# Kernel tuning notes

Measured on AMD Instinct MI355X. Metric: run time of the kernel, lower is better.

## Reference

```python
import jax, jax.numpy as jnp
import numpy as np

B_SZ, L, D_MODEL = 2, 2048, 2048
INTER, HEADS, P, N, G, K = 4096, 64, 64, 128, 1, 4
CONV_DIM = INTER + 2 * G * N
EPS = 1e-5


def silu(x):
    return x * jax.nn.sigmoid(x)


def softplus_thresh(x, threshold=10.0):
    # matches source: where(x < thr, log(1+exp(x)), x)
    return jnp.where(x < threshold, jnp.log1p(jnp.exp(jnp.minimum(x, threshold))), x)


def setup_inputs() -> dict:
    key = jax.random.key(0)
    ks = jax.random.split(key, 8)
    s = 0.02
    return {
        "hidden_states": jax.random.normal(ks[0], (B_SZ, L, D_MODEL), jnp.float32),
        "W_z": jax.random.normal(ks[1], (D_MODEL, INTER), jnp.float32) * s,
        "W_xBC": jax.random.normal(ks[2], (D_MODEL, CONV_DIM), jnp.float32) * s,
        "W_dt": jax.random.normal(ks[3], (D_MODEL, HEADS), jnp.float32) * s,
        "conv_w": jax.random.normal(ks[4], (CONV_DIM, K), jnp.float32) * 0.1,
        "conv_b": jnp.zeros((CONV_DIM,), jnp.float32),
        "dt_bias": jax.random.uniform(ks[5], (HEADS,), jnp.float32, -2.0, 0.0),
        "A_log": jnp.log(jnp.arange(1, HEADS + 1, dtype=jnp.float32)),
        "D": jnp.ones((HEADS,), jnp.float32),
        "norm_w": jnp.ones((INTER,), jnp.float32),
        "W_out": jax.random.normal(ks[6], (INTER, D_MODEL), jnp.float32) * s,
    }


def reference(hidden_states, W_z, W_xBC, W_dt, conv_w, conv_b, dt_bias, A_log, D, norm_w, W_out):
    b, l, _ = hidden_states.shape
    Hg = HEADS // G  # heads per group

    gate = hidden_states @ W_z                      # [b,l,INTER]
    xBC = hidden_states @ W_xBC                     # [b,l,CONV_DIM]
    dt = softplus_thresh(hidden_states @ W_dt + dt_bias)  # [b,l,H]

    # causal depthwise conv1d + silu (padding=K-1, truncated to seq_len)
    xp = jnp.pad(xBC, ((0, 0), (K - 1, 0), (0, 0)))
    kern = jnp.transpose(conv_w)[:, None, :]        # [K,1,CONV_DIM] (WIO)
    xBC = jax.lax.conv_general_dilated(
        xp, kern, (1,), 'VALID',
        dimension_numbers=('NWC', 'WIO', 'NWC'),
        feature_group_count=CONV_DIM)
    xBC = silu(xBC + conv_b)

    gns = G * N
    x = xBC[..., :INTER].reshape(b, l, G, Hg, P)
    Bm = xBC[..., INTER:INTER + gns].reshape(b, l, G, N)
    Cm = xBC[..., INTER + gns:].reshape(b, l, G, N)

    A = -jnp.exp(A_log)                             # [H]
    dA = jnp.exp(dt * A).reshape(b, l, G, Hg)       # [b,l,G,Hg]
    dtx = dt.reshape(b, l, G, Hg)[..., None] * x    # [b,l,G,Hg,P]

    def step(state, inp):
        dA_t, dtx_t, B_t, C_t = inp
        # state: [b,G,Hg,P,N]
        state = state * dA_t[..., None, None] + dtx_t[..., None] * B_t[:, :, None, None, :]
        y_t = jnp.einsum('bghpn,bgn->bghp', state, C_t)
        return state, y_t

    xs = (jnp.moveaxis(dA, 1, 0), jnp.moveaxis(dtx, 1, 0),
          jnp.moveaxis(Bm, 1, 0), jnp.moveaxis(Cm, 1, 0))
    state0 = jnp.zeros((b, G, Hg, P, N), jnp.float32)
    _, ys = jax.lax.scan(step, state0, xs)          # [l,b,G,Hg,P]
    y = jnp.moveaxis(ys, 0, 1) + D.reshape(G, Hg)[..., None] * x
    scan_out = y.reshape(b, l, INTER)

    # gated RMSNorm within groups
    hs = scan_out.reshape(b, l, G, INTER // G).astype(jnp.float32)
    gt = gate.reshape(b, l, G, INTER // G).astype(jnp.float32)
    hs = hs * silu(gt)
    var = jnp.mean(hs * hs, axis=-1, keepdims=True)
    hs = hs * jax.lax.rsqrt(var + EPS)
    normed = norm_w * hs.reshape(b, l, INTER)

    return normed @ W_out
```

## Files before the change

### kernel.cpp

```cpp
#include <hip/hip_runtime.h>
#include <hip/hip_bf16.h>
#include <math.h>

typedef unsigned short u16;
typedef unsigned int   u32;
typedef __attribute__((ext_vector_type(8))) short short8;
typedef __attribute__((ext_vector_type(4))) float f32x4;

#define B_SZ     2
#define LSEQ     2048
#define DMODEL   2048
#define INTER    4096
#define HEADS    64
#define NSTATE   128
#define CONV_DIM 4352
#define XSTR     8576
#define NFUSE    8704
#define EPS      1e-5f
#define QCH      64
#define NCHUNK   (LSEQ / QCH)

__device__ __forceinline__ float bf2f(u16 u) {
    u32 v = ((u32)u) << 16;
    return __builtin_bit_cast(float, v);
}
__device__ __forceinline__ u16 f2bf(float x) {
    __hip_bfloat16 h = __float2bfloat16(x);
    return __builtin_bit_cast(u16, h);
}
__device__ __forceinline__ u32 pack2(float lo, float hi) {
    return (u32)f2bf(lo) | ((u32)f2bf(hi) << 16);
}
__device__ __forceinline__ void gl2lds16(const void* g, void* l) {
    __builtin_amdgcn_global_load_lds(
        (const __attribute__((address_space(1))) u32*)g,
        (__attribute__((address_space(3))) u32*)l, 16, 0, 0);
}

__global__ __launch_bounds__(256) void cvt_f32_bf16(
    const float* __restrict__ in, u16* __restrict__ out, int n4)
{
    int i = blockIdx.x * 256 + threadIdx.x;
    if (i >= n4) return;
    float4 v = ((const float4*)in)[i];
    ushort4 o;
    o.x = f2bf(v.x); o.y = f2bf(v.y); o.z = f2bf(v.z); o.w = f2bf(v.w);
    ((ushort4*)out)[i] = o;
}

__global__ __launch_bounds__(256) void tr_f32_bf16(
    const float* __restrict__ in, u16* __restrict__ out, int R, int C)
{
    __shared__ u16 tile[64][68];
    const int r0 = blockIdx.y * 64, c0 = blockIdx.x * 64;
    const int tr = threadIdx.x >> 4, tc = (threadIdx.x & 15) * 4;
    #pragma unroll
    for (int i = 0; i < 4; ++i) {
        int r = tr + i * 16;
        float4 v = *(const float4*)(in + (size_t)(r0 + r) * C + c0 + tc);
        tile[r][tc + 0] = f2bf(v.x);
        tile[r][tc + 1] = f2bf(v.y);
        tile[r][tc + 2] = f2bf(v.z);
        tile[r][tc + 3] = f2bf(v.w);
    }
    __syncthreads();
    #pragma unroll
    for (int i = 0; i < 4; ++i) {
        int oc = tr + i * 16;
        ushort4 o;
        o.x = tile[tc + 0][oc];
        o.y = tile[tc + 1][oc];
        o.z = tile[tc + 2][oc];
        o.w = tile[tc + 3][oc];
        *(ushort4*)(out + (size_t)(c0 + oc) * R + r0 + tc) = o;
    }
}

#define SA(c) (smem + (c) * 32768)
#define SB(c) (smem + (c) * 32768 + 16384)
#define STGA(c, q, ko) gl2lds16(gA + (size_t)((q) * 64) * lda + (ko), SA(c) + (q) * 4096 + lbase)
#define STGB(c, q, ko) gl2lds16(gB + (size_t)((q) * 64) * ldb + (ko), SB(c) + (q) * 4096 + lbase)

#define PH(mh, kk, READB, STAGES, TAIL)                                          \
  {                                                                              \
    short8 af[4];                                                                \
    _Pragma("unroll")                                                            \
    for (int i_ = 0; i_ < 4; ++i_)                                               \
      af[i_] = *(const short8*)(Ab + (wm * 128 + (mh) * 64 + i_ * 16 + lr) * 64  \
                                + ((((kk) * 4 + lq) ^ (lr & 7)) << 3));          \
    if (READB) {                                                                 \
      _Pragma("unroll")                                                          \
      for (int j_ = 0; j_ < 4; ++j_)                                             \
        bfr[kk][j_] = *(const short8*)(Bb + (wn * 64 + j_ * 16 + lr) * 64        \
                                       + ((((kk) * 4 + lq) ^ (lr & 7)) << 3));   \
    }                                                                            \
    STAGES                                                                       \
    __builtin_amdgcn_sched_barrier(0);                                           \
    __builtin_amdgcn_s_barrier();                                                \
    asm volatile("s_waitcnt lgkmcnt(0)" ::: "memory");                           \
    __builtin_amdgcn_sched_barrier(0);                                           \
    __builtin_amdgcn_s_setprio(1);                                               \
    _Pragma("unroll")                                                            \
    for (int i_ = 0; i_ < 4; ++i_)                                               \
      _Pragma("unroll")                                                          \
      for (int j_ = 0; j_ < 4; ++j_)                                             \
        acc[(mh) * 4 + i_][j_] = __builtin_amdgcn_mfma_f32_16x16x32_bf16(        \
            af[i_], bfr[kk][j_], acc[(mh) * 4 + i_][j_], 0, 0, 0);               \
    __builtin_amdgcn_s_setprio(0);                                               \
    __builtin_amdgcn_sched_barrier(0);                                           \
    TAIL                                                                         \
    __builtin_amdgcn_s_barrier();                                                \
  }

#define TILE(tt, c)                                                              \
  {                                                                              \
    const int t_ = (tt);                                                         \
    const int k1_ = (t_ + 1) << 6, k2_ = (t_ + 2) << 6;                          \
    const bool st1_ = (t_ + 1 < nt), st2_ = (t_ + 2 < nt);                       \
    const u16* Ab = SA(c); const u16* Bb = SB(c);                                \
    PH(0, 0, 1, { if (st1_) { STGA((c) ^ 1, 1, k1_); STGA((c) ^ 1, 3, k1_); } }, {}) \
    PH(1, 0, 0, { if (st1_) { STGB((c) ^ 1, 0, k1_); STGB((c) ^ 1, 1, k1_); } }, {}) \
    PH(0, 1, 1, { if (st1_) { STGB((c) ^ 1, 2, k1_); STGB((c) ^ 1, 3, k1_); } }, {}) \
    PH(1, 1, 0, { if (st2_) { STGA((c), 0, k2_); STGA((c), 2, k2_); } },         \
       { if (t_ < nt - 1) {                                                      \
           if (st2_) { asm volatile("s_waitcnt vmcnt(2)" ::: "memory"); }        \
           else      { asm volatile("s_waitcnt vmcnt(0)" ::: "memory"); } } })   \
  }

template<int OUT_BF16>
__global__ __launch_bounds__(512, 2) void gemm8(
    const u16* __restrict__ A, const u16* __restrict__ Bt, void* __restrict__ Co,
    int K, int lda, int ldb, int ldc, int Nstore)
{
    __shared__ __align__(16) u16 smem[65536];
    const int tid  = threadIdx.x;
    const int wave = tid >> 6, lane = tid & 63;
    const int wm = wave >> 2, wn = wave & 3;
    const int lr = lane & 15, lq = lane >> 4;

    const int nbx = gridDim.x;
    const int bid = blockIdx.y * nbx + blockIdx.x;
    const int nwg = nbx * gridDim.y;
    const int cpx = nwg >> 3;
    const int swz = (bid & 7) * cpx + (bid >> 3);
    const int n0 = (swz % nbx) * 256;
    const int m0 = (swz / nbx) * 256;
    const int kbase = blockIdx.z * K;

    const int srow  = tid >> 3;
    const int scb8  = ((tid & 7) ^ (srow & 7)) << 3;
    const int lbase = (tid >> 6) << 9;
    const u16* gA = A  + (size_t)(m0 + srow) * lda + kbase + scb8;
    const u16* gB = Bt + (size_t)(n0 + srow) * ldb + kbase + scb8;

    f32x4 acc[8][4];
    #pragma unroll
    for (int i = 0; i < 8; ++i)
        #pragma unroll
        for (int j = 0; j < 4; ++j) acc[i][j] = (f32x4)0.f;
    short8 bfr[2][4];

    const int nt = K >> 6;

    STGA(0, 0, 0); STGA(0, 1, 0); STGA(0, 2, 0); STGA(0, 3, 0);
    STGB(0, 0, 0); STGB(0, 1, 0); STGB(0, 2, 0); STGB(0, 3, 0);
    STGA(1, 0, 64); STGA(1, 2, 64);
    __builtin_amdgcn_sched_barrier(0);
    asm volatile("s_waitcnt vmcnt(2)" ::: "memory");
    __builtin_amdgcn_sched_barrier(0);
    __builtin_amdgcn_s_barrier();

    for (int t = 0; t < nt; t += 2) {
        TILE(t, 0)
        TILE(t + 1, 1)
    }

    const int odd = lr & 1;
    const bool wstore = (n0 + wn * 64) < Nstore;
    #pragma unroll
    for (int i = 0; i < 8; ++i)
        #pragma unroll
        for (int j = 0; j < 4; ++j) {
            float v0 = acc[i][j][0], v1 = acc[i][j][1];
            float v2 = acc[i][j][2], v3 = acc[i][j][3];
            float n0v = __shfl_xor(v0, 1), n1v = __shfl_xor(v1, 1);
            float n2v = __shfl_xor(v2, 1), n3v = __shfl_xor(v3, 1);
            int colb  = n0 + wn * 64 + j * 16 + (lr & ~1);
            int rbase = m0 + wm * 128 + i * 16 + lq * 4 + odd * 2;
            if (wstore) {
                if (OUT_BF16) {
                    u32 w0 = odd ? pack2(n2v, v2) : pack2(v0, n0v);
                    u32 w1 = odd ? pack2(n3v, v3) : pack2(v1, n1v);
                    *(u32*)((u16*)Co + (size_t)rbase * ldc + colb) = w0;
                    *(u32*)((u16*)Co + (size_t)(rbase + 1) * ldc + colb) = w1;
                } else {
                    float* Cf = (float*)Co + (size_t)blockIdx.z * 4096 * ldc;
                    float2 f0 = odd ? make_float2(n2v, v2) : make_float2(v0, n0v);
                    float2 f1 = odd ? make_float2(n3v, v3) : make_float2(v1, n1v);
                    *(float2*)(Cf + (size_t)rbase * ldc + colb) = f0;
                    *(float2*)(Cf + (size_t)(rbase + 1) * ldc + colb) = f1;
                }
            }
        }
}

__global__ __launch_bounds__(256) void add2_f32(
    const float* __restrict__ a, const float* __restrict__ b,
    float* __restrict__ o, int n4)
{
    int i = blockIdx.x * 256 + threadIdx.x;
    if (i >= n4) return;
    float4 x = ((const float4*)a)[i];
    float4 y = ((const float4*)b)[i];
    x.x += y.x; x.y += y.y; x.z += y.z; x.w += y.w;
    ((float4*)o)[i] = x;
}

__global__ void dt_kernel(const u16* __restrict__ xall,
                          float* __restrict__ dtb,
                          const float* __restrict__ dt_bias, int n)
{
    int i = blockIdx.x * 256 + threadIdx.x;
    if (i >= n) return;
    int h = i & 63, row = i >> 6;
    float x = bf2f(xall[(size_t)row * XSTR + INTER + CONV_DIM + h]) + dt_bias[h];
    dtb[i] = (x < 10.f) ? log1pf(expf(x)) : x;
}

__global__ void conv_kernel(const u16* __restrict__ xall,
                            const float* __restrict__ cw,
                            const float* __restrict__ cb,
                            u16* __restrict__ xout)
{
    int c  = blockIdx.x * 256 + threadIdx.x;
    int bt = blockIdx.y;
    int t  = bt & (LSEQ - 1);
    const u16* xi = xall + (size_t)bt * XSTR + INTER + c;
    float4 w = *(const float4*)(cw + (size_t)c * 4);
    float acc = cb[c];
    acc = fmaf(bf2f(xi[0]), w.w, acc);
    if (t >= 1) acc = fmaf(bf2f(*(xi - XSTR)),     w.z, acc);
    if (t >= 2) acc = fmaf(bf2f(*(xi - 2 * XSTR)), w.y, acc);
    if (t >= 3) acc = fmaf(bf2f(*(xi - 3 * XSTR)), w.x, acc);
    xout[(size_t)bt * CONV_DIM + c] = f2bf(acc / (1.f + expf(-acc)));
}

__global__ __launch_bounds__(256) void ssd_chunk_state(
    const u16* __restrict__ xc, const float* __restrict__ dtb,
    const float* __restrict__ A_log,
    u16* __restrict__ Tg, float* __restrict__ decayQ)
{
    const int bid = blockIdx.x;
    const int b = bid >> 11, h = (bid >> 5) & 63, c = bid & 31;
    const int t0 = c * QCH;
    const int tid = threadIdx.x;
    const int wave = tid >> 6, lane = tid & 63;
    const int lr = lane & 15, lq = lane >> 4;

    __shared__ __align__(16) u16 BT[128][72];
    __shared__ __align__(16) u16 XwT[64][72];
    __shared__ float sclL[QCH];

    const u16* xg = xc + (size_t)b * LSEQ * CONV_DIM;

    if (tid < 64) {
        float dtv = dtb[((size_t)b * LSEQ + t0 + tid) * HEADS + h];
        float a = -dtv * expf(A_log[h]);
        float s = a;
        #pragma unroll
        for (int off = 1; off < 64; off <<= 1) {
            float o = __shfl_up(s, off, 64);
            if (tid >= off) s += o;
        }
        float cq = __shfl(s, 63, 64);
        sclL[tid] = dtv * expf(cq - s);
        if (tid == 0) decayQ[((b * 64 + h) << 5) + c] = expf(cq);
    }
    __syncthreads();

    #pragma unroll
    for (int r = 0; r < 16; ++r) {
        int idx = tid + 256 * r, j = idx >> 6, p = idx & 63;
        float v = bf2f(xg[(size_t)(t0 + j) * CONV_DIM + h * 64 + p]);
        XwT[p][j] = f2bf(v * sclL[j]);
    }
    #pragma unroll
    for (int r = 0; r < 32; ++r) {
        int idx = tid + 256 * r, j = idx >> 7, n = idx & 127;
        BT[n][j] = xg[(size_t)(t0 + j) * CONV_DIM + INTER + n];
    }
    __syncthreads();

    f32x4 acc[8];
    #pragma unroll
    for (int i = 0; i < 8; ++i) acc[i] = (f32x4)0.f;
    #pragma unroll
    for (int k0 = 0; k0 < QCH; k0 += 32) {
        short8 af = *(const short8*)&XwT[wave * 16 + lr][k0 + lq * 8];
        #pragma unroll
        for (int nt = 0; nt < 8; ++nt) {
            short8 bfr = *(const short8*)&BT[nt * 16 + lr][k0 + lq * 8];
            acc[nt] = __builtin_amdgcn_mfma_f32_16x16x32_bf16(af, bfr, acc[nt], 0, 0, 0);
        }
    }
    u16* To = Tg + ((((size_t)(b * 64 + h)) * NCHUNK + c) * 64) * 128;
    #pragma unroll
    for (int nt = 0; nt < 8; ++nt)
        #pragma unroll
        for (int r = 0; r < 4; ++r)
            To[(wave * 16 + lq * 4 + r) * 128 + nt * 16 + lr] = f2bf(acc[nt][r]);
}

__global__ __launch_bounds__(256) void ssd_state_scan(
    u16* __restrict__ Tg, const float* __restrict__ decayQ)
{
    const int bh = blockIdx.x, tid = threadIdx.x;
    const int p = tid >> 2, nb = (tid & 3) * 32;
    float S[32];
    #pragma unroll
    for (int m = 0; m < 32; ++m) S[m] = 0.f;

    for (int c = 0; c < NCHUNK; ++c) {
        u16* base = Tg + ((((size_t)bh * NCHUNK + c) * 64 + p) * 128) + nb;
        uint4 tv[4];
        #pragma unroll
        for (int k = 0; k < 4; ++k) tv[k] = *(const uint4*)(base + k * 8);
        #pragma unroll
        for (int k = 0; k < 4; ++k) {
            uint4 sv;
            sv.x = pack2(S[k*8+0], S[k*8+1]);
            sv.y = pack2(S[k*8+2], S[k*8+3]);
            sv.z = pack2(S[k*8+4], S[k*8+5]);
            sv.w = pack2(S[k*8+6], S[k*8+7]);
            *(uint4*)(base + k * 8) = sv;
        }
        float dq = decayQ[(bh << 5) + c];
        #pragma unroll
        for (int k = 0; k < 4; ++k) {
            const u32* w = (const u32*)&tv[k];
            #pragma unroll
            for (int e = 0; e < 4; ++e) {
                S[k*8 + e*2]     = fmaf(dq, S[k*8 + e*2],     bf2f((u16)(w[e] & 0xffffu)));
                S[k*8 + e*2 + 1] = fmaf(dq, S[k*8 + e*2 + 1], bf2f((u16)(w[e] >> 16)));
            }
        }
    }
}

__global__ __launch_bounds__(256) void ssd_output(
    const u16* __restrict__ xc, const float* __restrict__ dtb,
    const float* __restrict__ A_log, const float* __restrict__ Dvec,
    const u16* __restrict__ Sg,
    u16* __restrict__ y)
{
    const int bid = blockIdx.x;
    const int b = bid >> 11, h = (bid >> 5) & 63, c = bid & 31;
    const int t0 = c * QCH;
    const int tid = threadIdx.x;
    const int wave = tid >> 6, lane = tid & 63;
    const int lr = lane & 15, lq = lane >> 4;

    __shared__ __align__(16) u16 C_lds[64][136];
    __shared__ __align__(16) u16 B_lds[64][136];
    __shared__ __align__(16) u16 S_lds[64][136];
    __shared__ __align__(16) u16 P_lds[64][72];
    __shared__ __align__(16) u16 XT[64][72];
    __shared__ float cumL[QCH], dtsL[QCH], escL[QCH];

    const u16* xg = xc + (size_t)b * LSEQ * CONV_DIM;

    if (tid < 64) {
        float dtv = dtb[((size_t)b * LSEQ + t0 + tid) * HEADS + h];
        float a = -dtv * expf(A_log[h]);
        float s = a;
        #pragma unroll
        for (int off = 1; off < 64; off <<= 1) {
            float o = __shfl_up(s, off, 64);
            if (tid >= off) s += o;
        }
        cumL[tid] = s;
        dtsL[tid] = dtv;
        escL[tid] = expf(s);
    }
    #pragma unroll
    for (int r4 = 0; r4 < 4; ++r4) {
        int idx4 = tid + 256 * r4;
        int j = idx4 >> 4, c8 = (idx4 & 15) * 8;
        *(uint4*)&B_lds[j][c8] = *(const uint4*)(xg + (size_t)(t0 + j) * CONV_DIM + INTER + c8);
        *(uint4*)&C_lds[j][c8] = *(const uint4*)(xg + (size_t)(t0 + j) * CONV_DIM + INTER + NSTATE + c8);
        *(uint4*)&S_lds[j][c8] = *(const uint4*)(Sg + ((((size_t)(b * 64 + h)) * NCHUNK + c) * 64 + j) * 128 + c8);
    }
    #pragma unroll
    for (int r = 0; r < 16; ++r) {
        int idx = tid + 256 * r, j = idx >> 6, p = idx & 63;
        XT[p][j] = xg[(size_t)(t0 + j) * CONV_DIM + h * 64 + p];
    }
    __syncthreads();

    f32x4 accG[4];
    #pragma unroll
    for (int i = 0; i < 4; ++i) accG[i] = (f32x4)0.f;
    #pragma unroll
    for (int k0 = 0; k0 < NSTATE; k0 += 32) {
        short8 af = *(const short8*)&C_lds[wave * 16 + lr][k0 + lq * 8];
        #pragma unroll
        for (int jt = 0; jt < 4; ++jt) {
            short8 bfr = *(const short8*)&B_lds[jt * 16 + lr][k0 + lq * 8];
            accG[jt] = __builtin_amdgcn_mfma_f32_16x16x32_bf16(af, bfr, accG[jt], 0, 0, 0);
        }
    }
    #pragma unroll
    for (int jt = 0; jt < 4; ++jt)
        #pragma unroll
        for (int r = 0; r < 4; ++r) {
            int ii = wave * 16 + lq * 4 + r;
            int jj = jt * 16 + lr;
            float v = (jj <= ii)
                ? accG[jt][r] * dtsL[jj] * expf(cumL[ii] - cumL[jj]) : 0.f;
            P_lds[ii][jj] = f2bf(v);
        }
    __syncthreads();

    f32x4 accY[4], accZ[4];
    #pragma unroll
    for (int i = 0; i < 4; ++i) { accY[i] = (f32x4)0.f; accZ[i] = (f32x4)0.f; }
    #pragma unroll
    for (int k0 = 0; k0 < QCH; k0 += 32) {
        short8 af = *(const short8*)&P_lds[wave * 16 + lr][k0 + lq * 8];
        #pragma unroll
        for (int pt = 0; pt < 4; ++pt) {
            short8 bfr = *(const short8*)&XT[pt * 16 + lr][k0 + lq * 8];
            accY[pt] = __builtin_amdgcn_mfma_f32_16x16x32_bf16(af, bfr, accY[pt], 0, 0, 0);
        }
    }
    #pragma unroll
    for (int k0 = 0; k0 < NSTATE; k0 += 32) {
        short8 af = *(const short8*)&C_lds[wave * 16 + lr][k0 + lq * 8];
        #pragma unroll
        for (int pt = 0; pt < 4; ++pt) {
            short8 bfr = *(const short8*)&S_lds[pt * 16 + lr][k0 + lq * 8];
            accZ[pt] = __builtin_amdgcn_mfma_f32_16x16x32_bf16(af, bfr, accZ[pt], 0, 0, 0);
        }
    }

    const float Dh = Dvec[h];
    u16* yg = y + ((size_t)b * LSEQ + t0) * XSTR + h * 64;
    #pragma unroll
    for (int pt = 0; pt < 4; ++pt)
        #pragma unroll
        for (int r = 0; r < 4; ++r) {
            int ii = wave * 16 + lq * 4 + r;
            int pp = pt * 16 + lr;
            float xv = bf2f(XT[pp][ii]);
            float o = accY[pt][r] + escL[ii] * accZ[pt][r] + Dh * xv;
            yg[(size_t)ii * XSTR + pp] = f2bf(o);
        }
}

__global__ __launch_bounds__(256) void norm_kernel(
    u16* __restrict__ xall, const float* __restrict__ w)
{
    const int row = blockIdx.x;
    const u16* yr = xall + (size_t)row * XSTR + INTER;
    u16*       gr = xall + (size_t)row * XSTR;
    const int tid = threadIdx.x;

    float v[16];
    float ss = 0.f;
    #pragma unroll
    for (int i = 0; i < 16; ++i) {
        int idx = tid + i * 256;
        float hv = bf2f(yr[idx]);
        float g  = bf2f(gr[idx]);
        float val = hv * (g / (1.f + expf(-g)));
        v[i] = val;
        ss = fmaf(val, val, ss);
    }
    #pragma unroll
    for (int o = 32; o > 0; o >>= 1) ss += __shfl_xor(ss, o);
    __shared__ float part[4];
    if ((tid & 63) == 0) part[tid >> 6] = ss;
    __syncthreads();
    float tot  = part[0] + part[1] + part[2] + part[3];
    float rinv = rsqrtf(tot * (1.f / INTER) + EPS);
    #pragma unroll
    for (int i = 0; i < 16; ++i) {
        int idx = tid + i * 256;
        gr[idx] = f2bf(w[idx] * v[i] * rinv);
    }
}

extern "C" void kernel_launch(void* const* d_in, const int* in_sizes, int n_in,
                              void* d_out, int out_size, void* d_ws, size_t ws_size,
                              hipStream_t stream)
{
    const float* hs      = (const float*)d_in[0];
    const float* W_z     = (const float*)d_in[1];
    const float* W_xBC   = (const float*)d_in[2];
    const float* W_dt    = (const float*)d_in[3];
    const float* conv_w  = (const float*)d_in[4];
    const float* conv_b  = (const float*)d_in[5];
    const float* dt_bias = (const float*)d_in[6];
    const float* A_log   = (const float*)d_in[7];
    const float* Dv      = (const float*)d_in[8];
    const float* norm_w  = (const float*)d_in[9];
    const float* W_out   = (const float*)d_in[10];
    float* out = (float*)d_out;
    char*  w8  = (char*)d_ws;

    u16* hs_bf  = (u16*)(w8 + 0);
    u16* Wt_all = (u16*)(w8 + 16777216);
    u16* Tbuf   = (u16*)(w8 + 0);
    float* Cpart= (float*)(w8 + 0);
    u16* Wt_out = (u16*)(w8 + 67108864);
    u16* xall   = (u16*)(w8 + 83886080);
    u16* xconv  = (u16*)(w8 + 154140672);
    float* dtb  = (float*)(w8 + 189792256);
    float* dcq  = (float*)(w8 + 190840832);

    const int M = B_SZ * LSEQ;

    cvt_f32_bf16<<<(M * DMODEL / 4 + 255) / 256, 256, 0, stream>>>(hs, hs_bf, M * DMODEL / 4);
    tr_f32_bf16<<<dim3(INTER / 64,    DMODEL / 64), 256, 0, stream>>>(W_z,   Wt_all, DMODEL, INTER);
    tr_f32_bf16<<<dim3(CONV_DIM / 64, DMODEL / 64), 256, 0, stream>>>(W_xBC, Wt_all + (size_t)INTER * DMODEL, DMODEL, CONV_DIM);
    tr_f32_bf16<<<dim3(1,             DMODEL / 64), 256, 0, stream>>>(W_dt,  Wt_all + (size_t)(INTER + CONV_DIM) * DMODEL, DMODEL, 64);
    hipMemsetAsync(Wt_all + (size_t)(INTER + CONV_DIM + 64) * DMODEL, 0, (size_t)192 * DMODEL * 2, stream);
    tr_f32_bf16<<<dim3(DMODEL / 64,   INTER / 64),  256, 0, stream>>>(W_out, Wt_out, INTER, DMODEL);

    gemm8<1><<<dim3(NFUSE / 256, M / 256, 1), 512, 0, stream>>>(
        hs_bf, Wt_all, (void*)xall, DMODEL , DMODEL , DMODEL ,
        XSTR , XSTR );

    dt_kernel<<<(M * HEADS + 255) / 256, 256, 0, stream>>>(xall, dtb, dt_bias, M * HEADS);
    conv_kernel<<<dim3(CONV_DIM / 256, M), 256, 0, stream>>>(xall, conv_w, conv_b, xconv);

    ssd_chunk_state<<<B_SZ * HEADS * NCHUNK, 256, 0, stream>>>(xconv, dtb, A_log, Tbuf, dcq);
    ssd_state_scan<<<B_SZ * HEADS, 256, 0, stream>>>(Tbuf, dcq);
    ssd_output<<<B_SZ * HEADS * NCHUNK, 256, 0, stream>>>(xconv, dtb, A_log, Dv, Tbuf, xall + INTER);

    norm_kernel<<<M, 256, 0, stream>>>(xall, norm_w);

    gemm8<0><<<dim3(DMODEL / 256, M / 256, 2), 512, 0, stream>>>(
        xall, Wt_out, (void*)Cpart, INTER / 2 , XSTR ,
        INTER , DMODEL , DMODEL );
    add2_f32<<<(M * DMODEL / 4 + 255) / 256, 256, 0, stream>>>(
        Cpart, Cpart + (size_t)M * DMODEL, out, M * DMODEL / 4);
}
```

Baseline: 638.6 us.

## Replace 256x256x64 GEMM with 128x256x32 double-buffered kernel at higher occupancy

The two bf16 GEMMs move from a 256x256 tile with 64-wide K steps and a phased four-stage LDS pipeline to a 128x256 tile with 32-wide K steps. The new kernel uses a simple two-buffer LDS ring of 48KB and launch bounds allowing four blocks per CU. The aim is more resident waves and more blocks in flight to hide latency, at the cost of lower arithmetic intensity per tile and more barriers per unit of K. The XOR swizzle on LDS reads is dropped, which may bring bank conflicts back.

```diff
diff --git a/kernel.cpp b/kernel.cpp
--- a/kernel.cpp
+++ b/kernel.cpp
@@ -76,63 +76,12 @@
     }
 }
 
-#define SA(c) (smem + (c) * 32768)
-#define SB(c) (smem + (c) * 32768 + 16384)
-#define STGA(c, q, ko) gl2lds16(gA + (size_t)((q) * 64) * lda + (ko), SA(c) + (q) * 4096 + lbase)
-#define STGB(c, q, ko) gl2lds16(gB + (size_t)((q) * 64) * ldb + (ko), SB(c) + (q) * 4096 + lbase)
-
-#define PH(mh, kk, READB, STAGES, TAIL)                                          \
-  {                                                                              \
-    short8 af[4];                                                                \
-    _Pragma("unroll")                                                            \
-    for (int i_ = 0; i_ < 4; ++i_)                                               \
-      af[i_] = *(const short8*)(Ab + (wm * 128 + (mh) * 64 + i_ * 16 + lr) * 64  \
-                                + ((((kk) * 4 + lq) ^ (lr & 7)) << 3));          \
-    if (READB) {                                                                 \
-      _Pragma("unroll")                                                          \
-      for (int j_ = 0; j_ < 4; ++j_)                                             \
-        bfr[kk][j_] = *(const short8*)(Bb + (wn * 64 + j_ * 16 + lr) * 64        \
-                                       + ((((kk) * 4 + lq) ^ (lr & 7)) << 3));   \
-    }                                                                            \
-    STAGES                                                                       \
-    __builtin_amdgcn_sched_barrier(0);                                           \
-    __builtin_amdgcn_s_barrier();                                                \
-    asm volatile("s_waitcnt lgkmcnt(0)" ::: "memory");                           \
-    __builtin_amdgcn_sched_barrier(0);                                           \
-    __builtin_amdgcn_s_setprio(1);                                               \
-    _Pragma("unroll")                                                            \
-    for (int i_ = 0; i_ < 4; ++i_)                                               \
-      _Pragma("unroll")                                                          \
-      for (int j_ = 0; j_ < 4; ++j_)                                             \
-        acc[(mh) * 4 + i_][j_] = __builtin_amdgcn_mfma_f32_16x16x32_bf16(        \
-            af[i_], bfr[kk][j_], acc[(mh) * 4 + i_][j_], 0, 0, 0);               \
-    __builtin_amdgcn_s_setprio(0);                                               \
-    __builtin_amdgcn_sched_barrier(0);                                           \
-    TAIL                                                                         \
-    __builtin_amdgcn_s_barrier();                                                \
-  }
-
-#define TILE(tt, c)                                                              \
-  {                                                                              \
-    const int t_ = (tt);                                                         \
-    const int k1_ = (t_ + 1) << 6, k2_ = (t_ + 2) << 6;                          \
-    const bool st1_ = (t_ + 1 < nt), st2_ = (t_ + 2 < nt);                       \
-    const u16* Ab = SA(c); const u16* Bb = SB(c);                                \
-    PH(0, 0, 1, { if (st1_) { STGA((c) ^ 1, 1, k1_); STGA((c) ^ 1, 3, k1_); } }, {}) \
-    PH(1, 0, 0, { if (st1_) { STGB((c) ^ 1, 0, k1_); STGB((c) ^ 1, 1, k1_); } }, {}) \
-    PH(0, 1, 1, { if (st1_) { STGB((c) ^ 1, 2, k1_); STGB((c) ^ 1, 3, k1_); } }, {}) \
-    PH(1, 1, 0, { if (st2_) { STGA((c), 0, k2_); STGA((c), 2, k2_); } },         \
-       { if (t_ < nt - 1) {                                                      \
-           if (st2_) { asm volatile("s_waitcnt vmcnt(2)" ::: "memory"); }        \
-           else      { asm volatile("s_waitcnt vmcnt(0)" ::: "memory"); } } })   \
-  }
-
 template<int OUT_BF16>
-__global__ __launch_bounds__(512, 2) void gemm8(
+__global__ __launch_bounds__(512, 4) void gemmk(
     const u16* __restrict__ A, const u16* __restrict__ Bt, void* __restrict__ Co,
     int K, int lda, int ldb, int ldc, int Nstore)
 {
-    __shared__ __align__(16) u16 smem[65536];
+    __shared__ __align__(16) u16 smem[2][12288];
     const int tid  = threadIdx.x;
     const int wave = tid >> 6, lane = tid & 63;
     const int wm = wave >> 2, wn = wave & 3;
@@ -144,41 +93,86 @@
     const int cpx = nwg >> 3;
     const int swz = (bid & 7) * cpx + (bid >> 3);
     const int n0 = (swz % nbx) * 256;
-    const int m0 = (swz / nbx) * 256;
+    const int m0 = (swz / nbx) * 128;
     const int kbase = blockIdx.z * K;
 
-    const int srow  = tid >> 3;
-    const int scb8  = ((tid & 7) ^ (srow & 7)) << 3;
-    const int lbase = (tid >> 6) << 9;
-    const u16* gA = A  + (size_t)(m0 + srow) * lda + kbase + scb8;
-    const u16* gB = Bt + (size_t)(n0 + srow) * ldb + kbase + scb8;
-
-    f32x4 acc[8][4];
-    #pragma unroll
-    for (int i = 0; i < 8; ++i)
+    const int lbase = wave << 9;
+    const u16* gA = A  + (size_t)(m0 + (tid >> 2)) * lda + kbase + (tid & 3) * 8;
+    const u16* gB = Bt + (size_t)(n0 + (tid >> 2)) * ldb + kbase + (tid & 3) * 8;
+
+    f32x4 acc[4][4];
+    #pragma unroll
+    for (int i = 0; i < 4; ++i)
         #pragma unroll
         for (int j = 0; j < 4; ++j) acc[i][j] = (f32x4)0.f;
-    short8 bfr[2][4];
-
-    const int nt = K >> 6;
-
-    STGA(0, 0, 0); STGA(0, 1, 0); STGA(0, 2, 0); STGA(0, 3, 0);
-    STGB(0, 0, 0); STGB(0, 1, 0); STGB(0, 2, 0); STGB(0, 3, 0);
-    STGA(1, 0, 64); STGA(1, 2, 64);
+
+    const int nt = K >> 5;
+
+    gl2lds16(gA,                  &smem[0][0]    + lbase);
+    gl2lds16(gB,                  &smem[0][4096] + lbase);
+    gl2lds16(gB + (size_t)128 * ldb, &smem[0][8192] + lbase);
+    gl2lds16(gA + 32,                &smem[1][0]    + lbase);
+    gl2lds16(gB + 32,                &smem[1][4096] + lbase);
+    gl2lds16(gB + (size_t)128 * ldb + 32, &smem[1][8192] + lbase);
     __builtin_amdgcn_sched_barrier(0);
-    asm volatile("s_waitcnt vmcnt(2)" ::: "memory");
+    asm volatile("s_waitcnt vmcnt(3)" ::: "memory");
     __builtin_amdgcn_sched_barrier(0);
     __builtin_amdgcn_s_barrier();
 
-    for (int t = 0; t < nt; t += 2) {
-        TILE(t, 0)
-        TILE(t + 1, 1)
+    const u16* gA2 = gA + 64;
+    const u16* gB2 = gB + 64;
+
+    for (int t = 0; t < nt; ++t) {
+        const int c = t & 1;
+        const u16* Ab = &smem[c][0];
+        const u16* Bb = &smem[c][4096];
+        short8 af0 = *(const short8*)(Ab + (wm * 64 +  0 + lr) * 32 + lq * 8);
+        short8 af1 = *(const short8*)(Ab + (wm * 64 + 16 + lr) * 32 + lq * 8);
+        short8 bfr[4];
+        #pragma unroll
+        for (int j = 0; j < 4; ++j)
+            bfr[j] = *(const short8*)(Bb + (wn * 64 + j * 16 + lr) * 32 + lq * 8);
+        short8 af2 = *(const short8*)(Ab + (wm * 64 + 32 + lr) * 32 + lq * 8);
+        short8 af3 = *(const short8*)(Ab + (wm * 64 + 48 + lr) * 32 + lq * 8);
+        __builtin_amdgcn_s_setprio(1);
+        #pragma unroll
+        for (int j = 0; j < 4; ++j) {
+            acc[0][j] = __builtin_amdgcn_mfma_f32_16x16x32_bf16(af0, bfr[j], acc[0][j], 0, 0, 0);
+            acc[1][j] = __builtin_amdgcn_mfma_f32_16x16x32_bf16(af1, bfr[j], acc[1][j], 0, 0, 0);
+        }
+        __builtin_amdgcn_s_setprio(0);
+        asm volatile("s_waitcnt lgkmcnt(0)" ::: "memory");
+        __builtin_amdgcn_sched_barrier(0);
+        __builtin_amdgcn_s_barrier();
+
+        const bool st2 = (t + 2 < nt);
+        if (st2) {
+            gl2lds16(gA2,                  &smem[c][0]    + lbase);
+            gl2lds16(gB2,                  &smem[c][4096] + lbase);
+            gl2lds16(gB2 + (size_t)128 * ldb, &smem[c][8192] + lbase);
+            gA2 += 32; gB2 += 32;
+        }
+        __builtin_amdgcn_sched_barrier(0);
+        __builtin_amdgcn_s_setprio(1);
+        #pragma unroll
+        for (int j = 0; j < 4; ++j) {
+            acc[2][j] = __builtin_amdgcn_mfma_f32_16x16x32_bf16(af2, bfr[j], acc[2][j], 0, 0, 0);
+            acc[3][j] = __builtin_amdgcn_mfma_f32_16x16x32_bf16(af3, bfr[j], acc[3][j], 0, 0, 0);
+        }
+        __builtin_amdgcn_s_setprio(0);
+        __builtin_amdgcn_sched_barrier(0);
+        if (st2) {
+            asm volatile("s_waitcnt vmcnt(3)" ::: "memory");
+        } else if (t + 1 < nt) {
+            asm volatile("s_waitcnt vmcnt(0)" ::: "memory");
+        }
+        __builtin_amdgcn_s_barrier();
     }
 
     const int odd = lr & 1;
     const bool wstore = (n0 + wn * 64) < Nstore;
     #pragma unroll
-    for (int i = 0; i < 8; ++i)
+    for (int i = 0; i < 4; ++i)
         #pragma unroll
         for (int j = 0; j < 4; ++j) {
             float v0 = acc[i][j][0], v1 = acc[i][j][1];
@@ -186,7 +180,7 @@
             float n0v = __shfl_xor(v0, 1), n1v = __shfl_xor(v1, 1);
             float n2v = __shfl_xor(v2, 1), n3v = __shfl_xor(v3, 1);
             int colb  = n0 + wn * 64 + j * 16 + (lr & ~1);
-            int rbase = m0 + wm * 128 + i * 16 + lq * 4 + odd * 2;
+            int rbase = m0 + wm * 64 + i * 16 + lq * 4 + odd * 2;
             if (wstore) {
                 if (OUT_BF16) {
                     u32 w0 = odd ? pack2(n2v, v2) : pack2(v0, n0v);
@@ -527,7 +521,7 @@
     hipMemsetAsync(Wt_all + (size_t)(INTER + CONV_DIM + 64) * DMODEL, 0, (size_t)192 * DMODEL * 2, stream);
     tr_f32_bf16<<<dim3(DMODEL / 64,   INTER / 64),  256, 0, stream>>>(W_out, Wt_out, INTER, DMODEL);
 
-    gemm8<1><<<dim3(NFUSE / 256, M / 256, 1), 512, 0, stream>>>(
+    gemmk<1><<<dim3(NFUSE / 256, M / 128, 1), 512, 0, stream>>>(
         hs_bf, Wt_all, (void*)xall, DMODEL , DMODEL , DMODEL ,
         XSTR , XSTR );
 
@@ -540,7 +534,7 @@
 
     norm_kernel<<<M, 256, 0, stream>>>(xall, norm_w);
 
-    gemm8<0><<<dim3(DMODEL / 256, M / 256, 2), 512, 0, stream>>>(
+    gemmk<0><<<dim3(DMODEL / 256, M / 128, 2), 512, 0, stream>>>(
         xall, Wt_out, (void*)Cpart, INTER / 2 , XSTR ,
         INTER , DMODEL , DMODEL );
     add2_f32<<<(M * DMODEL / 4 + 255) / 256, 256, 0, stream>>>(
```

Result: slower. 672.1 us (+5.2%).

## Split-K the projection GEMM tail and parallelize state scan across N quarters

Applied to the files above, without the earlier changes.

The fused input-projection GEMM is split into a main 8192-column part and a 512-column tail. The tail (the last xBC, dt and padding columns) runs as a 4-way split-K fp32 GEMM and is reduced into bf16 by a new tail_add kernel, which is meant to cut the wave-quantization cost of the partial last column tile. Separately, ssd_state_scan now launches 4x more blocks, each handling 8 state elements per thread instead of 32, to expose more parallelism in the sequential chunk scan. The change adds two extra launches and an fp32 partial buffer that aliases the xconv region.

```diff
diff --git a/kernel.cpp b/kernel.cpp
--- a/kernel.cpp
+++ b/kernel.cpp
@@ -15,7 +15,9 @@
 #define NSTATE   128
 #define CONV_DIM 4352
 #define XSTR     8576
-#define NFUSE    8704
+#define NMAIN    8192
+#define NTAILC   512
+#define NTAILS   384
 #define EPS      1e-5f
 #define QCH      64
 #define NCHUNK   (LSEQ / QCH)
@@ -204,6 +206,25 @@
         }
 }
 
+__global__ __launch_bounds__(256) void tail_add(
+    const float* __restrict__ Pt, u16* __restrict__ xall_)
+{
+    int i = blockIdx.x * 256 + threadIdx.x;
+    int row = i / 96, cq = (i % 96) * 4;
+    const float* p = Pt + (size_t)row * NTAILC + cq;
+    const size_t zs = (size_t)4096 * NTAILC;
+    float4 a = *(const float4*)(p);
+    float4 b = *(const float4*)(p + zs);
+    float4 c = *(const float4*)(p + 2 * zs);
+    float4 d = *(const float4*)(p + 3 * zs);
+    ushort4 o;
+    o.x = f2bf(a.x + b.x + c.x + d.x);
+    o.y = f2bf(a.y + b.y + c.y + d.y);
+    o.z = f2bf(a.z + b.z + c.z + d.z);
+    o.w = f2bf(a.w + b.w + c.w + d.w);
+    *(ushort4*)(xall_ + (size_t)row * XSTR + NMAIN + cq) = o;
+}
+
 __global__ __launch_bounds__(256) void add2_f32(
     const float* __restrict__ a, const float* __restrict__ b,
     float* __restrict__ o, int n4)
@@ -314,35 +335,28 @@
 __global__ __launch_bounds__(256) void ssd_state_scan(
     u16* __restrict__ Tg, const float* __restrict__ decayQ)
 {
-    const int bh = blockIdx.x, tid = threadIdx.x;
-    const int p = tid >> 2, nb = (tid & 3) * 32;
-    float S[32];
-    #pragma unroll
-    for (int m = 0; m < 32; ++m) S[m] = 0.f;
+    const int bh = blockIdx.x >> 2, nq = blockIdx.x & 3;
+    const int tid = threadIdx.x;
+    const int p = tid >> 2, nb = nq * 32 + (tid & 3) * 8;
+    float S[8];
+    #pragma unroll
+    for (int m = 0; m < 8; ++m) S[m] = 0.f;
 
     for (int c = 0; c < NCHUNK; ++c) {
         u16* base = Tg + ((((size_t)bh * NCHUNK + c) * 64 + p) * 128) + nb;
-        uint4 tv[4];
-        #pragma unroll
-        for (int k = 0; k < 4; ++k) tv[k] = *(const uint4*)(base + k * 8);
-        #pragma unroll
-        for (int k = 0; k < 4; ++k) {
-            uint4 sv;
-            sv.x = pack2(S[k*8+0], S[k*8+1]);
-            sv.y = pack2(S[k*8+2], S[k*8+3]);
-            sv.z = pack2(S[k*8+4], S[k*8+5]);
-            sv.w = pack2(S[k*8+6], S[k*8+7]);
-            *(uint4*)(base + k * 8) = sv;
-        }
+        uint4 tv = *(const uint4*)base;
+        uint4 sv;
+        sv.x = pack2(S[0], S[1]);
+        sv.y = pack2(S[2], S[3]);
+        sv.z = pack2(S[4], S[5]);
+        sv.w = pack2(S[6], S[7]);
+        *(uint4*)base = sv;
         float dq = decayQ[(bh << 5) + c];
-        #pragma unroll
-        for (int k = 0; k < 4; ++k) {
-            const u32* w = (const u32*)&tv[k];
-            #pragma unroll
-            for (int e = 0; e < 4; ++e) {
-                S[k*8 + e*2]     = fmaf(dq, S[k*8 + e*2],     bf2f((u16)(w[e] & 0xffffu)));
-                S[k*8 + e*2 + 1] = fmaf(dq, S[k*8 + e*2 + 1], bf2f((u16)(w[e] >> 16)));
-            }
+        const u32* w = (const u32*)&tv;
+        #pragma unroll
+        for (int e = 0; e < 4; ++e) {
+            S[e*2]     = fmaf(dq, S[e*2],     bf2f((u16)(w[e] & 0xffffu)));
+            S[e*2 + 1] = fmaf(dq, S[e*2 + 1], bf2f((u16)(w[e] >> 16)));
         }
     }
 }
@@ -515,6 +529,7 @@
     u16* Wt_out = (u16*)(w8 + 67108864);
     u16* xall   = (u16*)(w8 + 83886080);
     u16* xconv  = (u16*)(w8 + 154140672);
+    float* Ptail= (float*)(w8 + 154140672);
     float* dtb  = (float*)(w8 + 189792256);
     float* dcq  = (float*)(w8 + 190840832);
 
@@ -527,15 +542,19 @@
     hipMemsetAsync(Wt_all + (size_t)(INTER + CONV_DIM + 64) * DMODEL, 0, (size_t)192 * DMODEL * 2, stream);
     tr_f32_bf16<<<dim3(DMODEL / 64,   INTER / 64),  256, 0, stream>>>(W_out, Wt_out, INTER, DMODEL);
 
-    gemm8<1><<<dim3(NFUSE / 256, M / 256, 1), 512, 0, stream>>>(
-        hs_bf, Wt_all, (void*)xall, DMODEL , DMODEL , DMODEL ,
-        XSTR , XSTR );
+    gemm8<1><<<dim3(NMAIN / 256, M / 256, 1), 512, 0, stream>>>(
+        hs_bf, Wt_all, (void*)xall, DMODEL , DMODEL, DMODEL,
+        XSTR , NMAIN );
+    gemm8<0><<<dim3(NTAILC / 256, M / 256, 4), 512, 0, stream>>>(
+        hs_bf, Wt_all + (size_t)NMAIN * DMODEL, (void*)Ptail, DMODEL / 4 ,
+        DMODEL, DMODEL, NTAILC , NTAILS );
+    tail_add<<<M * (NTAILS / 4) / 256, 256, 0, stream>>>(Ptail, xall);
 
     dt_kernel<<<(M * HEADS + 255) / 256, 256, 0, stream>>>(xall, dtb, dt_bias, M * HEADS);
     conv_kernel<<<dim3(CONV_DIM / 256, M), 256, 0, stream>>>(xall, conv_w, conv_b, xconv);
 
     ssd_chunk_state<<<B_SZ * HEADS * NCHUNK, 256, 0, stream>>>(xconv, dtb, A_log, Tbuf, dcq);
-    ssd_state_scan<<<B_SZ * HEADS, 256, 0, stream>>>(Tbuf, dcq);
+    ssd_state_scan<<<B_SZ * HEADS * 4, 256, 0, stream>>>(Tbuf, dcq);
     ssd_output<<<B_SZ * HEADS * NCHUNK, 256, 0, stream>>>(xconv, dtb, A_log, Dv, Tbuf, xall + INTER);
 
     norm_kernel<<<M, 256, 0, stream>>>(xall, norm_w);
```

Measured after the change: 610.5 us. -4.4%, faster.
